# Optimization experiments

Hardware: AMD Instinct MI355X
Metric: run time of the kernel (lower is better)

Reference implementation:

```python
import jax, jax.numpy as jnp
import numpy as np

# Dimensions per init_kwargs
B, S, D = 2, 2048, 1024          # batch, seq, hidden_size
F = 4096                          # intermediate_size
E, K = 8, 2                       # moe_num_experts, moe_top_k
EPS = 1e-9


def setup_inputs() -> dict:
    key = jax.random.key(0)
    k1, k2, k3, k4 = jax.random.split(key, 4)
    x = jax.random.normal(k1, (B, S, D), dtype=jnp.float32)
    # gate: Linear(D, E, bias=False) -> stored as [D, E] for x @ w_gate
    w_gate = jax.random.normal(k2, (D, E), dtype=jnp.float32) * 0.02
    # per-expert gate_up_proj: Linear(D, 2F, bias=False), stacked over experts -> [E, D, 2F]
    w_gate_up = jax.random.normal(k3, (E, D, 2 * F), dtype=jnp.float32) * 0.02
    # per-expert down_proj: Linear(F, D, bias=False), stacked -> [E, F, D]
    w_down = jax.random.normal(k4, (E, F, D), dtype=jnp.float32) * 0.02
    return {"x": x, "w_gate": w_gate, "w_gate_up": w_gate_up, "w_down": w_down}


def reference(x, w_gate, w_gate_up, w_down):
    # Router
    gate_logits = x @ w_gate                       # [B,S,E]
    gate_probs = jax.nn.softmax(gate_logits, axis=-1)
    # top-k masking + renormalization (top_k < num_experts)
    topk_vals, topk_idx = jax.lax.top_k(gate_probs, K)           # [B,S,K]
    masked = jnp.sum(jax.nn.one_hot(topk_idx, E, dtype=gate_probs.dtype)
                     * topk_vals[..., None], axis=-2)            # [B,S,E]
    denom = jnp.maximum(jnp.sum(masked, axis=-1, keepdims=True), EPS)
    gate_probs = masked / denom

    # Dense per-expert SwiGLU FFN on all tokens (faithful to reference impl)
    gu = jnp.einsum('bsd,edh->ebsh', x, w_gate_up)               # [E,B,S,2F]
    g, u = jnp.split(gu, 2, axis=-1)                             # [E,B,S,F] each
    act = jax.nn.silu(g) * u                                     # [E,B,S,F]
    expert_out = jnp.einsum('ebsf,efd->ebsd', act, w_down)       # [E,B,S,D]

    # Gate-weighted combine
    return jnp.einsum('bse,ebsd->bsd', gate_probs, expert_out)   # [B,S,D]
```

## Files before the change

### kernel.cpp

```cpp
#include <hip/hip_runtime.h>
#include <stdint.h>

#define NTOK 4096
#define DMODEL 1024
#define FF 4096
#define NEXP 8

typedef __bf16 bf16x8 __attribute__((ext_vector_type(8)));
typedef float f32x4 __attribute__((ext_vector_type(4)));
typedef unsigned short u16x8 __attribute__((ext_vector_type(8)));

__device__ __forceinline__ unsigned short f2bf(float f) {
  union { float f; unsigned u; } v; v.f = f;
  unsigned r = v.u + 0x7fffu + ((v.u >> 16) & 1u);
  return (unsigned short)(r >> 16);
}

__global__ __launch_bounds__(256) void k_convert_x(const float4* __restrict__ in,
                                                   ushort4* __restrict__ out, int n4) {
  int stride = gridDim.x * blockDim.x;
  for (int i = blockIdx.x * blockDim.x + threadIdx.x; i < n4; i += stride) {
    float4 v = in[i];
    out[i] = make_ushort4(f2bf(v.x), f2bf(v.y), f2bf(v.z), f2bf(v.w));
  }
}

__global__ __launch_bounds__(256) void k_transpose_bf16(const float* __restrict__ in,
                                                        unsigned short* __restrict__ out,
                                                        int R, int C) {
  __shared__ float tile[64][65];
  const size_t slab = (size_t)R * C;
  const float* ip = in + slab * blockIdx.z;
  unsigned short* op = out + slab * blockIdx.z;
  int c0 = blockIdx.x * 64, r0 = blockIdx.y * 64;
  int tx = threadIdx.x & 15, ty = threadIdx.x >> 4;
#pragma unroll
  for (int i = 0; i < 4; ++i) {
    int r = ty + 16 * i;
    float4 v = *(const float4*)(ip + (size_t)(r0 + r) * C + c0 + tx * 4);
    tile[r][tx * 4 + 0] = v.x;
    tile[r][tx * 4 + 1] = v.y;
    tile[r][tx * 4 + 2] = v.z;
    tile[r][tx * 4 + 3] = v.w;
  }
  __syncthreads();
  int w = threadIdx.x >> 6, lane = threadIdx.x & 63;
  int rc = (lane & 7) * 8;
#pragma unroll
  for (int pass = 0; pass < 2; ++pass) {
    int c = pass * 32 + w * 8 + (lane >> 3);
    u16x8 o;
#pragma unroll
    for (int j = 0; j < 8; ++j) o[j] = f2bf(tile[rc + j][c]);
    *(u16x8*)(op + (size_t)(c0 + c) * R + r0 + rc) = o;
  }
}

__global__ __launch_bounds__(256) void k_router(const float* __restrict__ x,
                                                const float* __restrict__ wg,
                                                int* __restrict__ cnt,
                                                int* __restrict__ elist,
                                                float* __restrict__ gw) {
  int wave = threadIdx.x >> 6, lane = threadIdx.x & 63;
  int t = blockIdx.x * 4 + wave;
  const float* xp = x + (size_t)t * DMODEL;
  float a[8] = {0, 0, 0, 0, 0, 0, 0, 0};
#pragma unroll
  for (int i = 0; i < DMODEL / 64; ++i) {
    int d = lane + 64 * i;
    float xv = xp[d];
    float4 w0 = *(const float4*)(wg + d * 8);
    float4 w1 = *(const float4*)(wg + d * 8 + 4);
    a[0] += xv * w0.x; a[1] += xv * w0.y; a[2] += xv * w0.z; a[3] += xv * w0.w;
    a[4] += xv * w1.x; a[5] += xv * w1.y; a[6] += xv * w1.z; a[7] += xv * w1.w;
  }
#pragma unroll
  for (int off = 32; off > 0; off >>= 1)
#pragma unroll
    for (int e = 0; e < 8; ++e) a[e] += __shfl_down(a[e], off, 64);
  if (lane == 0) {
    int e0 = 0;
    for (int e = 1; e < 8; ++e) if (a[e] > a[e0]) e0 = e;
    int e1 = (e0 == 0) ? 1 : 0;
    for (int e = 0; e < 8; ++e) if (e != e0 && a[e] > a[e1]) e1 = e;
    float p = __expf(a[e1] - a[e0]);
    float inv = 1.0f / (1.0f + p);
    int p0 = atomicAdd(&cnt[e0], 1);
    elist[e0 * NTOK + p0] = 2 * t;
    gw[2 * t] = inv;
    int p1 = atomicAdd(&cnt[e1], 1);
    elist[e1 * NTOK + p1] = 2 * t + 1;
    gw[2 * t + 1] = p * inv;
  }
}

__global__ __launch_bounds__(512, 4) void k_gemm1(const unsigned short* __restrict__ xb,
                                                  const unsigned short* __restrict__ wgu,
                                                  const int* __restrict__ cnt,
                                                  const int* __restrict__ elist,
                                                  unsigned short* __restrict__ act)
{
  __shared__ __align__(16) unsigned short sA[2][128 * 64];
  __shared__ __align__(16) unsigned short sB[2][128 * 64];

  const int e = blockIdx.z;
  const int n_e = cnt[e];
  const int m0 = blockIdx.y * 128;
  if (m0 >= n_e) return;
  const int c0 = blockIdx.x * 64;
  int abase = 0;
#pragma unroll
  for (int j = 0; j < NEXP; ++j) abase += (j < e) ? cnt[j] : 0;
  const int tid = threadIdx.x;
  const int w = tid >> 6, lane = tid & 63;
  const int wr = w >> 2, wc = w & 3;
  const int* el = elist + e * NTOK;
  const int csub = ((lane & 7) ^ (lane >> 3)) * 8;
  const int srow = w * 8 + (lane >> 3);

  int tokrow[2];
  size_t baddr[2];
  const unsigned short* wb = wgu + (size_t)e * (2 * FF) * DMODEL;
#pragma unroll
  for (int i = 0; i < 2; ++i) {
    int r = i * 64 + srow;
    int idx = m0 + r;
    tokrow[i] = el[idx < n_e ? idx : 0] >> 1;
    int strip = r >> 5, off = r & 31;
    int wrow = (off < 16) ? (c0 + strip * 16 + off) : (FF + c0 + strip * 16 + off - 16);
    baddr[i] = (size_t)wrow * DMODEL;
  }

  f32x4 acc[4][2];
  f32x4 zero = {0.f, 0.f, 0.f, 0.f};
#pragma unroll
  for (int m = 0; m < 4; ++m)
#pragma unroll
    for (int n = 0; n < 2; ++n) acc[m][n] = zero;

  auto stage = [&](int buf, int k0) {
#pragma unroll
    for (int i = 0; i < 2; ++i) {
      const unsigned short* g2 = xb + (size_t)tokrow[i] * DMODEL + k0 + csub;
      __builtin_amdgcn_global_load_lds((const __attribute__((address_space(1))) void*)g2,
                                       (__attribute__((address_space(3))) void*)(&sA[buf][(i * 64 + w * 8) * 64]),
                                       16, 0, 0);
    }
#pragma unroll
    for (int i = 0; i < 2; ++i) {
      const unsigned short* g2 = wb + baddr[i] + k0 + csub;
      __builtin_amdgcn_global_load_lds((const __attribute__((address_space(1))) void*)g2,
                                       (__attribute__((address_space(3))) void*)(&sB[buf][(i * 64 + w * 8) * 64]),
                                       16, 0, 0);
    }
  };

  auto compute = [&](int buf) {
#pragma unroll
    for (int kk = 0; kk < 2; ++kk) {
      const int xk = ((kk * 4 + (lane >> 4)) ^ (lane & 7)) * 8;
      bf16x8 af[4], bf[2];
#pragma unroll
      for (int m = 0; m < 4; ++m)
        af[m] = *(const bf16x8*)(&sA[buf][(wr * 64 + m * 16 + (lane & 15)) * 64 + xk]);
#pragma unroll
      for (int n = 0; n < 2; ++n)
        bf[n] = *(const bf16x8*)(&sB[buf][(wc * 32 + n * 16 + (lane & 15)) * 64 + xk]);
#pragma unroll
      for (int m = 0; m < 4; ++m)
#pragma unroll
        for (int n = 0; n < 2; ++n)
          acc[m][n] = __builtin_amdgcn_mfma_f32_16x16x32_bf16(af[m], bf[n], acc[m][n], 0, 0, 0);
    }
  };

  stage(0, 0);
  __syncthreads();
  int cur = 0;
  for (int t = 0; t < DMODEL / 64; ++t) {
    if (t + 1 < DMODEL / 64) stage(cur ^ 1, (t + 1) * 64);
    compute(cur);
    __syncthreads();
    cur ^= 1;
  }

#pragma unroll
  for (int m = 0; m < 4; ++m) {
#pragma unroll
    for (int r = 0; r < 4; ++r) {
      int idx = m0 + wr * 64 + m * 16 + (lane >> 4) * 4 + r;
      if (idx < n_e) {
        unsigned short* ap = act + (size_t)(abase + idx) * FF + c0 + wc * 16;
        float gv = acc[m][0][r];
        float u = acc[m][1][r];
        float s = gv / (1.0f + __expf(-gv));
        ap[lane & 15] = f2bf(s * u);
      }
    }
  }
}

__global__ __launch_bounds__(512, 2) void k_gemm2(const unsigned short* __restrict__ actb,
                                                  const unsigned short* __restrict__ wd,
                                                  const int* __restrict__ cnt,
                                                  const int* __restrict__ elist,
                                                  const float* __restrict__ gw,
                                                  float* __restrict__ out)
{
  __shared__ __align__(16) unsigned short sA[128 * 64];
  __shared__ __align__(16) unsigned short sB[256 * 64];

  const int bid = blockIdx.x;
  const int orig = (bid & 7) * 128 + (bid >> 3);
  const int g = orig >> 5;
  const int y = orig & 31;
  const int e = g >> 2;
  const int n_e = cnt[e];
  const int m0 = y * 128;
  if (m0 >= n_e) return;
  const int n0 = (g & 3) * 256;
  int abase = 0;
#pragma unroll
  for (int j = 0; j < NEXP; ++j) abase += (j < e) ? cnt[j] : 0;
  const int tid = threadIdx.x;
  const int w = tid >> 6, lane = tid & 63;
  const int wr = w >> 2, wc = w & 3;
  const int* el = elist + e * NTOK;
  const int csub = ((lane & 7) ^ (lane >> 3)) * 8;
  const int srow = w * 8 + (lane >> 3);

  int arow[2];
  size_t baddr[4];
  const unsigned short* wb = wd + (size_t)e * DMODEL * FF;
#pragma unroll
  for (int i = 0; i < 2; ++i) {
    int r = m0 + i * 64 + srow;
    arow[i] = abase + (r < n_e ? r : 0);
  }
#pragma unroll
  for (int j = 0; j < 4; ++j)
    baddr[j] = (size_t)(n0 + j * 64 + srow) * FF;

  f32x4 acc[4][4];
  f32x4 zero = {0.f, 0.f, 0.f, 0.f};
#pragma unroll
  for (int m = 0; m < 4; ++m)
#pragma unroll
    for (int n = 0; n < 4; ++n) acc[m][n] = zero;

  for (int k0 = 0; k0 < FF; k0 += 64) {
#pragma unroll
    for (int i = 0; i < 2; ++i) {
      const unsigned short* g2 = actb + (size_t)arow[i] * FF + k0 + csub;
      __builtin_amdgcn_global_load_lds((const __attribute__((address_space(1))) void*)g2,
                                       (__attribute__((address_space(3))) void*)(&sA[(i * 64 + w * 8) * 64]),
                                       16, 0, 0);
    }
#pragma unroll
    for (int j = 0; j < 4; ++j) {
      const unsigned short* g2 = wb + baddr[j] + k0 + csub;
      __builtin_amdgcn_global_load_lds((const __attribute__((address_space(1))) void*)g2,
                                       (__attribute__((address_space(3))) void*)(&sB[(j * 64 + w * 8) * 64]),
                                       16, 0, 0);
    }
    __syncthreads();
#pragma unroll
    for (int kk = 0; kk < 2; ++kk) {
      const int xk = ((kk * 4 + (lane >> 4)) ^ (lane & 7)) * 8;
      bf16x8 af[4], bf[4];
#pragma unroll
      for (int m = 0; m < 4; ++m)
        af[m] = *(const bf16x8*)(&sA[(wr * 64 + m * 16 + (lane & 15)) * 64 + xk]);
#pragma unroll
      for (int n = 0; n < 4; ++n)
        bf[n] = *(const bf16x8*)(&sB[(wc * 64 + n * 16 + (lane & 15)) * 64 + xk]);
#pragma unroll
      for (int m = 0; m < 4; ++m)
#pragma unroll
        for (int n = 0; n < 4; ++n)
          acc[m][n] = __builtin_amdgcn_mfma_f32_16x16x32_bf16(af[m], bf[n], acc[m][n], 0, 0, 0);
    }
    __syncthreads();
  }

#pragma unroll
  for (int m = 0; m < 4; ++m) {
#pragma unroll
    for (int r = 0; r < 4; ++r) {
      int idx = m0 + wr * 64 + m * 16 + (lane >> 4) * 4 + r;
      if (idx < n_e) {
        int p = el[idx];
        float wgt = gw[p];
        float* op = out + (size_t)(p >> 1) * DMODEL + n0 + wc * 64;
#pragma unroll
        for (int n = 0; n < 4; ++n)
          atomicAdd(&op[n * 16 + (lane & 15)], acc[m][n][r] * wgt);
      }
    }
  }
}

extern "C" void kernel_launch(void* const* d_in, const int* in_sizes, int n_in,
                              void* d_out, int out_size, void* d_ws, size_t ws_size,
                              hipStream_t stream) {
  const float* x   = (const float*)d_in[0];
  const float* wg  = (const float*)d_in[1];
  const float* wgu = (const float*)d_in[2];
  const float* wd  = (const float*)d_in[3];
  float* out = (float*)d_out;

  char* ws = (char*)d_ws;
  size_t off = 0;
  auto alloc = [&](size_t bytes) -> char* {
    char* p = ws + off;
    off += (bytes + 255) & ~(size_t)255;
    return p;
  };
  unsigned short* wgu_t = (unsigned short*)alloc((size_t)NEXP * 2 * FF * DMODEL * 2);
  unsigned short* wd_t  = (unsigned short*)alloc((size_t)NEXP * DMODEL * FF * 2);
  unsigned short* actb  = (unsigned short*)alloc((size_t)2 * NTOK * FF * 2);
  unsigned short* xb    = (unsigned short*)alloc((size_t)NTOK * DMODEL * 2);
  int* elist            = (int*)alloc((size_t)NEXP * NTOK * 4);
  float* gw             = (float*)alloc((size_t)2 * NTOK * 4);
  int* cnt              = (int*)alloc(256);
  if (off > ws_size) return;

  hipMemsetAsync(cnt, 0, 256, stream);
  hipMemsetAsync(out, 0, (size_t)NTOK * DMODEL * 4, stream);
  k_convert_x<<<1024, 256, 0, stream>>>((const float4*)x, (ushort4*)xb, NTOK * DMODEL / 4);
  k_transpose_bf16<<<dim3(2 * FF / 64, DMODEL / 64, NEXP), 256, 0, stream>>>(wgu, wgu_t, DMODEL, 2 * FF);
  k_transpose_bf16<<<dim3(DMODEL / 64, FF / 64, NEXP), 256, 0, stream>>>(wd, wd_t, FF, DMODEL);
  k_router<<<NTOK / 4, 256, 0, stream>>>(x, wg, cnt, elist, gw);
  k_gemm1<<<dim3(FF / 64, NTOK / 128, NEXP), 512, 0, stream>>>(xb, wgu_t, cnt, elist, actb);
  k_gemm2<<<1024, 512, 0, stream>>>(actb, wd_t, cnt, elist, gw, out);
}
```

Measured before the change: 566.5 us.

## Split gemm2 K dimension four ways with smaller 128x128 tiles

The down-projection GEMM now uses 256-thread blocks with 128x128 output tiles and splits the 4096-long reduction into four 1024-wide chunks. The grid grows from 1024 to 8192 blocks, interleaved by expert. The aim is more parallelism and better occupancy, since many tiles return early when an expert has few tokens. The cost is four partial results per output element that must be combined, presumably with atomic adds into the zeroed output, which adds atomic traffic and reads the A tiles more often.

```diff
diff --git a/kernel.cpp b/kernel.cpp
--- a/kernel.cpp
+++ b/kernel.cpp
@@ -200,7 +200,7 @@
   }
 }
 
-__global__ __launch_bounds__(512, 2) void k_gemm2(const unsigned short* __restrict__ actb,
+__global__ __launch_bounds__(256, 4) void k_gemm2(const unsigned short* __restrict__ actb,
                                                   const unsigned short* __restrict__ wd,
                                                   const int* __restrict__ cnt,
                                                   const int* __restrict__ elist,
@@ -208,38 +208,37 @@
                                                   float* __restrict__ out)
 {
   __shared__ __align__(16) unsigned short sA[128 * 64];
-  __shared__ __align__(16) unsigned short sB[256 * 64];
+  __shared__ __align__(16) unsigned short sB[128 * 64];
 
   const int bid = blockIdx.x;
-  const int orig = (bid & 7) * 128 + (bid >> 3);
-  const int g = orig >> 5;
-  const int y = orig & 31;
-  const int e = g >> 2;
+  const int e = bid & 7;
+  const int within = bid >> 3;
+  const int kc = within >> 8;
+  const int y = (within >> 3) & 31;
+  const int xcol = within & 7;
   const int n_e = cnt[e];
   const int m0 = y * 128;
   if (m0 >= n_e) return;
-  const int n0 = (g & 3) * 256;
+  const int n0 = xcol * 128;
   int abase = 0;
 #pragma unroll
   for (int j = 0; j < NEXP; ++j) abase += (j < e) ? cnt[j] : 0;
   const int tid = threadIdx.x;
   const int w = tid >> 6, lane = tid & 63;
-  const int wr = w >> 2, wc = w & 3;
+  const int wr = w >> 1, wc = w & 1;
   const int* el = elist + e * NTOK;
   const int csub = ((lane & 7) ^ (lane >> 3)) * 8;
-  const int srow = w * 8 + (lane >> 3);
-
-  int arow[2];
+
+  int arow[4];
   size_t baddr[4];
   const unsigned short* wb = wd + (size_t)e * DMODEL * FF;
 #pragma unroll
-  for (int i = 0; i < 2; ++i) {
-    int r = m0 + i * 64 + srow;
-    arow[i] = abase + (r < n_e ? r : 0);
-  }
-#pragma unroll
-  for (int j = 0; j < 4; ++j)
-    baddr[j] = (size_t)(n0 + j * 64 + srow) * FF;
+  for (int i = 0; i < 4; ++i) {
+    int r = i * 32 + w * 8 + (lane >> 3);
+    int idx = m0 + r;
+    arow[i] = abase + (idx < n_e ? idx : 0);
+    baddr[i] = (size_t)(n0 + r) * FF;
+  }
 
   f32x4 acc[4][4];
   f32x4 zero = {0.f, 0.f, 0.f, 0.f};
@@ -248,19 +247,20 @@
 #pragma unroll
     for (int n = 0; n < 4; ++n) acc[m][n] = zero;
 
-  for (int k0 = 0; k0 < FF; k0 += 64) {
-#pragma unroll
-    for (int i = 0; i < 2; ++i) {
+  const int kbeg = kc * 1024, kend = kbeg + 1024;
+  for (int k0 = kbeg; k0 < kend; k0 += 64) {
+#pragma unroll
+    for (int i = 0; i < 4; ++i) {
       const unsigned short* g2 = actb + (size_t)arow[i] * FF + k0 + csub;
       __builtin_amdgcn_global_load_lds((const __attribute__((address_space(1))) void*)g2,
-                                       (__attribute__((address_space(3))) void*)(&sA[(i * 64 + w * 8) * 64]),
+                                       (__attribute__((address_space(3))) void*)(&sA[(i * 32 + w * 8) * 64]),
                                        16, 0, 0);
     }
 #pragma unroll
-    for (int j = 0; j < 4; ++j) {
-      const unsigned short* g2 = wb + baddr[j] + k0 + csub;
+    for (int i = 0; i < 4; ++i) {
+      const unsigned short* g2 = wb + baddr[i] + k0 + csub;
       __builtin_amdgcn_global_load_lds((const __attribute__((address_space(1))) void*)g2,
-                                       (__attribute__((address_space(3))) void*)(&sB[(j * 64 + w * 8) * 64]),
+                                       (__attribute__((address_space(3))) void*)(&sB[(i * 32 + w * 8) * 64]),
                                        16, 0, 0);
     }
     __syncthreads();
@@ -332,5 +332,5 @@
   k_transpose_bf16<<<dim3(DMODEL / 64, FF / 64, NEXP), 256, 0, stream>>>(wd, wd_t, FF, DMODEL);
   k_router<<<NTOK / 4, 256, 0, stream>>>(x, wg, cnt, elist, gw);
   k_gemm1<<<dim3(FF / 64, NTOK / 128, NEXP), 512, 0, stream>>>(xb, wgu_t, cnt, elist, actb);
-  k_gemm2<<<1024, 512, 0, stream>>>(actb, wd_t, cnt, elist, gw, out);
-}
+  k_gemm2<<<8192, 256, 0, stream>>>(actb, wd_t, cnt, elist, gw, out);
+}
```

New measurement: 582.2 us. 2.8% more time.
